# Kernel optimization log

Hardware: AMD Instinct MI355X
Metric: run time of the kernel (lower is better)

## Reference

```python
import jax, jax.numpy as jnp
import numpy as np

B, C, T, COLS = 256, 1, 128, 512
IN_DIM = C * COLS          # 512
EMB = 1024
HID = 1024
NUM_LAYERS = 2
NUM_CLASSES = 10


def setup_inputs() -> dict:
    key = jax.random.key(0)
    ks = jax.random.split(key, 16)
    s = 0.05
    inp = {
        "x": jax.random.normal(ks[0], (B, C, T, COLS), dtype=jnp.float32),
        "W_enc": jax.random.normal(ks[1], (EMB, IN_DIM), dtype=jnp.float32) * s,
        "b_enc": jnp.zeros((EMB,), dtype=jnp.float32),
        # layer 0: input size EMB
        "W_ih0": jax.random.normal(ks[2], (4 * HID, EMB), dtype=jnp.float32) * s,
        "W_hh0": jax.random.normal(ks[3], (4 * HID, HID), dtype=jnp.float32) * s,
        "b_ih0": jnp.zeros((4 * HID,), dtype=jnp.float32),
        "b_hh0": jnp.zeros((4 * HID,), dtype=jnp.float32),
        # layer 1: input size HID
        "W_ih1": jax.random.normal(ks[4], (4 * HID, HID), dtype=jnp.float32) * s,
        "W_hh1": jax.random.normal(ks[5], (4 * HID, HID), dtype=jnp.float32) * s,
        "b_ih1": jnp.zeros((4 * HID,), dtype=jnp.float32),
        "b_hh1": jnp.zeros((4 * HID,), dtype=jnp.float32),
        "W_cls": jax.random.normal(ks[6], (NUM_CLASSES, HID), dtype=jnp.float32) * s,
        "b_cls": jnp.zeros((NUM_CLASSES,), dtype=jnp.float32),
    }
    return inp


def _lstm_cell(x, h, c, W_ih, W_hh, b_ih, b_hh):
    # gates: [B, 4H], PyTorch gate order i, f, g, o
    gates = x @ W_ih.T + b_ih + h @ W_hh.T + b_hh
    i, f, g, o = jnp.split(gates, 4, axis=-1)
    i = jax.nn.sigmoid(i)
    f = jax.nn.sigmoid(f)
    g = jnp.tanh(g)
    o = jax.nn.sigmoid(o)
    c_new = f * c + i * g
    h_new = o * jnp.tanh(c_new)
    return h_new, c_new


def reference(x, W_enc, b_enc, W_ih0, W_hh0, b_ih0, b_hh0,
              W_ih1, W_hh1, b_ih1, b_hh1, W_cls, b_cls):
    b_size = x.shape[0]
    # [B, C, T, COLS] -> [B, T, C*COLS]
    x_rowed = x.reshape(b_size, T, IN_DIM)
    emb = x_rowed @ W_enc.T + b_enc            # [B, T, EMB]
    emb_t = jnp.transpose(emb, (1, 0, 2))      # [T, B, EMB]

    layer_params = [(W_ih0, W_hh0, b_ih0, b_hh0), (W_ih1, W_hh1, b_ih1, b_hh1)]
    h0 = jnp.zeros((NUM_LAYERS, b_size, HID), dtype=x.dtype)
    c0 = jnp.zeros((NUM_LAYERS, b_size, HID), dtype=x.dtype)

    def step(carry, x_t):
        h, c = carry  # each [L, B, H]
        inp = x_t
        hs, cs = [], []
        for l in range(NUM_LAYERS):
            h_l, c_l = _lstm_cell(inp, h[l], c[l], *layer_params[l])
            hs.append(h_l)
            cs.append(c_l)
            inp = h_l
        return (jnp.stack(hs), jnp.stack(cs)), inp

    (_, _), outs = jax.lax.scan(step, (h0, c0), emb_t)  # outs: [T, B, H]
    last = outs[-1]                                     # [B, H]
    y = last @ W_cls.T + b_cls                          # [B, 10]
    return y
```

## Files before the change

kernel.cpp:

```cpp
#include <hip/hip_runtime.h>

#define B_SZ   256
#define T_SZ   128
#define IN_DIM 512
#define EMB    1024
#define HID    1024
#define G4     4096
#define NCLS   10
#define PSTR   2560
#define NBLK   256

typedef __attribute__((ext_vector_type(8))) short short8v;
typedef __attribute__((ext_vector_type(4))) float floatx4;

__device__ __forceinline__ unsigned short bf16hi(float f) {
    union { float f; unsigned u; } v; v.f = f;
    unsigned r = v.u + 0x7fff + ((v.u >> 16) & 1);
    return (unsigned short)(r >> 16);
}
__device__ __forceinline__ float bf2f(unsigned short b) {
    union { unsigned u; float f; } v; v.u = ((unsigned)b) << 16;
    return v.f;
}

#define LGKM0_BAR()  do { \
    asm volatile("s_waitcnt lgkmcnt(0)" ::: "memory"); \
    __builtin_amdgcn_sched_barrier(0); \
    __builtin_amdgcn_s_barrier(); \
    __builtin_amdgcn_sched_barrier(0); } while (0)

template<int BM,int BN,int BK,int TM,int TN>
__global__ __launch_bounds__((BM/TM)*(BN/TN))
void gemm_f32_nn(const float* __restrict__ A, const float* __restrict__ Bm,
                 float* __restrict__ C, int M, int N, int K) {
    constexpr int THREADS = (BM/TM)*(BN/TN);
    __shared__ float As[BK][BM+4];
    __shared__ float Bs[BK][BN+4];
    const int tid  = threadIdx.x;
    const int tcol = tid % (BN/TN);
    const int trow = tid / (BN/TN);
    const int bm   = blockIdx.y * BM;
    const int bn   = blockIdx.x * BN;
    float acc[TM][TN];
#pragma unroll
    for (int i = 0; i < TM; ++i)
#pragma unroll
        for (int j = 0; j < TN; ++j) acc[i][j] = 0.f;
    for (int k0 = 0; k0 < K; k0 += BK) {
#pragma unroll
        for (int r = 0; r < BM*BK/4; r += THREADS) {
            int i  = r + tid;
            int m  = i / (BK/4);
            int kk = (i % (BK/4)) * 4;
            const float4 v = *(const float4*)(&A[(size_t)(bm+m)*K + k0 + kk]);
            As[kk+0][m]=v.x; As[kk+1][m]=v.y; As[kk+2][m]=v.z; As[kk+3][m]=v.w;
        }
#pragma unroll
        for (int r = 0; r < BK*BN/4; r += THREADS) {
            int i  = r + tid;
            int kk = i / (BN/4);
            int n4 = (i % (BN/4)) * 4;
            const float4 v = *(const float4*)(&Bm[(size_t)(k0+kk)*N + bn + n4]);
            *(float4*)(&Bs[kk][n4]) = v;
        }
        __syncthreads();
#pragma unroll
        for (int k = 0; k < BK; ++k) {
            float a[TM], b[TN];
#pragma unroll
            for (int i = 0; i < TM; ++i) a[i] = As[k][trow*TM+i];
#pragma unroll
            for (int j = 0; j < TN; ++j) b[j] = Bs[k][tcol*TN+j];
#pragma unroll
            for (int i = 0; i < TM; ++i)
#pragma unroll
                for (int j = 0; j < TN; ++j) acc[i][j] += a[i]*b[j];
        }
        __syncthreads();
    }
#pragma unroll
    for (int i = 0; i < TM; ++i)
#pragma unroll
        for (int j = 0; j < TN; ++j)
            C[(size_t)(bm+trow*TM+i)*N + bn + tcol*TN + j] = acc[i][j];
}

__global__ void swz2(const float* __restrict__ M0, int K0, int kf0,
                     const float* __restrict__ M1, int K1, int kfcnt,
                     unsigned short* __restrict__ dst) {
    int gid = blockIdx.x * 256 + threadIdx.x;
    int l   = gid & 63;
    int kf  = (gid >> 6) % kfcnt;
    int cf  = gid / (64 * kfcnt);
    int n   = cf*16 + (l & 15);
    int row = ((n & 3) << 10) + (n >> 2);
    const float* src; int kk = (l >> 4) * 8;
    if (kf < kf0) { src = M0 + (size_t)row * K0; kk += kf * 32; }
    else          { src = M1 + (size_t)row * K1; kk += (kf - kf0) * 32; }
    short8v vh, vl;
#pragma unroll
    for (int j = 0; j < 8; ++j) {
        float f = src[kk + j];
        unsigned short h = bf16hi(f);
        vh[j] = (short)h;
        vl[j] = (short)bf16hi(f - bf2f(h));
    }
    size_t base = ((size_t)(cf * kfcnt + kf) * 2) * 512 + (size_t)l * 8;
    *(short8v*)(dst + base)       = vh;
    *(short8v*)(dst + base + 512) = vl;
}

__global__ void build_bcombI(const float* __restrict__ W_ih0, const float* __restrict__ b_enc,
                             const float* __restrict__ b_ih0, const float* __restrict__ b_hh0,
                             float* __restrict__ bcombI) {
    int row  = blockIdx.x * 4 + (threadIdx.x >> 6);
    int lane = threadIdx.x & 63;
    const float* w = W_ih0 + (size_t)row * EMB;
    float s = 0.f;
    for (int k = lane; k < EMB; k += 64) s += w[k] * b_enc[k];
#pragma unroll
    for (int o = 32; o > 0; o >>= 1) s += __shfl_down(s, o);
    if (lane == 0) {
        int n = ((row & 1023) << 2) | (row >> 10);
        bcombI[n] = s + b_ih0[row] + b_hh0[row];
    }
}

__global__ void addvI(const float* __restrict__ a, const float* __restrict__ b,
                      float* __restrict__ o) {
    int i = blockIdx.x * 256 + threadIdx.x;
    int n = ((i & 1023) << 2) | (i >> 10);
    o[n] = a[i] + b[i];
}

__device__ __forceinline__ void gridbar(unsigned* bar, unsigned target, int tid) {
    __syncthreads();
    if (tid == 0) {
        __threadfence();
        atomicAdd(bar, 1u);
        while (__hip_atomic_load(bar, __ATOMIC_RELAXED, __HIP_MEMORY_SCOPE_AGENT) < target)
            __builtin_amdgcn_s_sleep(1);
        __threadfence();
    }
    __syncthreads();
}

__device__ __forceinline__ void store_xz(unsigned short* ph, unsigned short* pl,
                                         int bid, int tid, float2 xv) {
    unsigned short h0 = bf16hi(xv.x), h1 = bf16hi(xv.y);
    ushort2 hh; hh.x = h0; hh.y = h1;
    ushort2 lv; lv.x = bf16hi(xv.x - bf2f(h0)); lv.y = bf16hi(xv.y - bf2f(h1));
    size_t o = (size_t)bid * PSTR + tid * 2;
    *(ushort2*)(ph + o) = hh;
    *(ushort2*)(pl + o) = lv;
}

__global__ __launch_bounds__(512, 1)
void lstm_persist(const float* __restrict__ x,
                  const unsigned short* __restrict__ WLz,
                  const unsigned short* __restrict__ WRz,
                  const float* __restrict__ biasLI, const float* __restrict__ biasRI,
                  unsigned short* __restrict__ p0h, unsigned short* __restrict__ p0l,
                  unsigned short* __restrict__ p1h, unsigned short* __restrict__ p1l,
                  const float* __restrict__ Wcls, const float* __restrict__ bcls,
                  float* __restrict__ out, unsigned* __restrict__ bar) {
    __shared__ unsigned short AslH[32768];
    float (*gtile)[68] = (float (*)[68])AslH;

    const int tid = threadIdx.x, bid = blockIdx.x;
    const int w = tid >> 6, l = tid & 63;
    const int kgrp = w >> 2, sub = w & 3;
    const int rowhalf = sub & 1, colhalf = sub >> 1;
    const int xcd = bid & 7;
    const int idx = bid >> 3;
    const bool is_left = (idx < 16);
    const int i2 = is_left ? idx : idx - 16;
    const int cgl = xcd * 8 + (i2 & 7);
    const int rg  = i2 >> 3;
    const int kfcnt = is_left ? 48 : 64;
    const int SMAXH = is_left ? 24 : 32;
    const int acol0 = is_left ? 0 : 512;
    const int hcol0 = is_left ? 512 : 1536;
    const int r0 = rg * 128;
    const unsigned short* Bz = is_left ? WLz : WRz;
    const float* biasI = is_left ? biasLI : biasRI;
    const int kf_base = kgrp * SMAXH;
    const int NS = SMAXH;

    const int cf0 = cgl*4 + colhalf*2;
    const unsigned short* bp0 = Bz + ((size_t)cf0     * kfcnt) * 1024 + (size_t)l * 8;
    const unsigned short* bp1 = Bz + ((size_t)(cf0+1) * kfcnt) * 1024 + (size_t)l * 8;

    float bias0 = 0.f, bias1 = 0.f;
    if (kgrp == 0) {
        int cA = cgl*64 + colhalf*32 + (l & 15);
        bias0 = biasI[cA]; bias1 = biasI[cA + 16];
    }

    unsigned short* PH[2] = {p0h, p1h};
    unsigned short* PL[2] = {p0l, p1l};

    float cst[4];
#pragma unroll
    for (int i = 0; i < 4; ++i) cst[i] = 0.f;

    unsigned target = 0;

    if (tid < 256) {
        float2 xv = *(const float2*)&x[((size_t)bid * T_SZ) * IN_DIM + tid * 2];
        store_xz(p0h, p0l, bid, tid, xv);
    }
    target += NBLK; gridbar(bar, target, tid);

    for (int t = 0; t <= T_SZ; ++t) {
        const int cur = t & 1, nxt = cur ^ 1;
        const bool conv = (t < T_SZ - 1) && (tid < 256);
        float2 xv;
        if (conv) xv = *(const float2*)&x[((size_t)bid * T_SZ + t + 1) * IN_DIM + tid * 2];

        const bool active = is_left ? (t < T_SZ) : (t >= 1);
        if (active) {
            const unsigned short* ph  = PH[cur];
            const unsigned short* plo = PL[cur];

            auto loadA = [&](int s, short8v (&r)[4]) {
#pragma unroll
                for (int i = 0; i < 4; ++i) {
                    int seg = w*4 + i;
                    int kg = seg >> 4, mf = (seg >> 1) & 7, pl = seg & 1;
                    int kf = kg * SMAXH + s;
                    const unsigned short* p = pl ? plo : ph;
                    size_t o = (size_t)(r0 + mf*16 + (l & 15)) * PSTR
                             + acol0 + kf*32 + ((l >> 4) * 8);
                    r[i] = *(const short8v*)(p + o);
                }
            };
            auto writeA = [&](int buf, short8v (&r)[4]) {
#pragma unroll
                for (int i = 0; i < 4; ++i) {
                    int seg = w*4 + i;
                    int kg = seg >> 4, mf = (seg >> 1) & 7, pl = seg & 1;
                    *(short8v*)(AslH + (size_t)((((buf*2 + kg)*8 + mf)*2 + pl)*64 + l)*8) = r[i];
                }
            };
            auto loadB = [&](int s, short8v (&b)[4]) {
                int kf = kf_base + s;
                const unsigned short* q0 = bp0 + (size_t)kf * 1024;
                const unsigned short* q1 = bp1 + (size_t)kf * 1024;
                b[0] = *(const short8v*)q0; b[1] = *(const short8v*)(q0 + 512);
                b[2] = *(const short8v*)q1; b[3] = *(const short8v*)(q1 + 512);
            };

            floatx4 acc[4][2];
#pragma unroll
            for (int m = 0; m < 4; ++m) {
                acc[m][0] = (floatx4){bias0, bias0, bias0, bias0};
                acc[m][1] = (floatx4){bias1, bias1, bias1, bias1};
            }

            auto mfmaStage = [&](int buf, short8v (&b)[4]) {
                short8v ah[4], al[4];
#pragma unroll
                for (int m = 0; m < 4; ++m) {
                    size_t base = (size_t)((((buf*2 + kgrp)*8 + rowhalf*4 + m)*2)*64 + l)*8;
                    ah[m] = *(const short8v*)(AslH + base);
                    al[m] = *(const short8v*)(AslH + base + 512);
                }
#pragma unroll
                for (int m = 0; m < 4; ++m) {
                    acc[m][0] = __builtin_amdgcn_mfma_f32_16x16x32_bf16(ah[m], b[0], acc[m][0], 0, 0, 0);
                    acc[m][0] = __builtin_amdgcn_mfma_f32_16x16x32_bf16(ah[m], b[1], acc[m][0], 0, 0, 0);
                    acc[m][0] = __builtin_amdgcn_mfma_f32_16x16x32_bf16(al[m], b[0], acc[m][0], 0, 0, 0);
                    acc[m][1] = __builtin_amdgcn_mfma_f32_16x16x32_bf16(ah[m], b[2], acc[m][1], 0, 0, 0);
                    acc[m][1] = __builtin_amdgcn_mfma_f32_16x16x32_bf16(ah[m], b[3], acc[m][1], 0, 0, 0);
                    acc[m][1] = __builtin_amdgcn_mfma_f32_16x16x32_bf16(al[m], b[2], acc[m][1], 0, 0, 0);
                }
            };

            short8v rA[4], rB[4], bE[4], bO[4];
            loadA(0, rA); loadB(0, bE);
            loadA(1, rB); loadB(1, bO);
            writeA(0, rA);
            LGKM0_BAR();

            for (int s = 0; s < NS; s += 2) {
                if (s + 2 < NS) loadA(s + 2, rA);
                writeA(1, rB);
                mfmaStage(0, bE);
                if (s + 2 < NS) loadB(s + 2, bE);
                LGKM0_BAR();
                if (s + 3 < NS) loadA(s + 3, rB);
                if (s + 2 < NS) writeA(0, rA);
                mfmaStage(1, bO);
                if (s + 3 < NS) loadB(s + 3, bO);
                LGKM0_BAR();
            }
            __syncthreads();

            if (kgrp == 0) {
#pragma unroll
                for (int m = 0; m < 4; ++m)
#pragma unroll
                    for (int c = 0; c < 2; ++c) {
                        int col = colhalf*32 + c*16 + (l & 15);
#pragma unroll
                        for (int jj = 0; jj < 4; ++jj)
                            gtile[rowhalf*64 + m*16 + ((l >> 4)*4) + jj][col] = acc[m][c][jj];
                    }
            }
            __syncthreads();
            if (kgrp == 1) {
#pragma unroll
                for (int m = 0; m < 4; ++m)
#pragma unroll
                    for (int c = 0; c < 2; ++c) {
                        int col = colhalf*32 + c*16 + (l & 15);
#pragma unroll
                        for (int jj = 0; jj < 4; ++jj)
                            gtile[rowhalf*64 + m*16 + ((l >> 4)*4) + jj][col] += acc[m][c][jj];
                    }
            }
            __syncthreads();

            {
                int u = tid & 15, rq = tid >> 4;
                unsigned short* nh = PH[nxt];
                unsigned short* nl = PL[nxt];
#pragma unroll
                for (int i = 0; i < 4; ++i) {
                    int r = rq*4 + i;
                    float4 gq = *(const float4*)&gtile[r][4*u];
                    float ii = 1.f / (1.f + expf(-gq.x));
                    float ff = 1.f / (1.f + expf(-gq.y));
                    float gg = tanhf(gq.z);
                    float oo = 1.f / (1.f + expf(-gq.w));
                    float cn = ff * cst[i] + ii * gg;
                    cst[i] = cn;
                    float h = oo * tanhf(cn);
                    unsigned short hh = bf16hi(h);
                    size_t o = (size_t)(r0 + r) * PSTR + hcol0 + cgl*16 + u;
                    nh[o] = hh;
                    nl[o] = bf16hi(h - bf2f(hh));
                }
            }
        }

        if (conv) store_xz(PH[nxt], PL[nxt], bid, tid, xv);
        target += NBLK; gridbar(bar, target, tid);
    }

    {
        const unsigned short* hh = PH[(T_SZ + 1) & 1];
        const unsigned short* hl = PL[(T_SZ + 1) & 1];
        float part[NCLS];
#pragma unroll
        for (int n = 0; n < NCLS; ++n) part[n] = 0.f;
        for (int k = tid; k < HID; k += 512) {
            size_t o = (size_t)bid * PSTR + 1536 + k;
            float hv = bf2f(hh[o]) + bf2f(hl[o]);
#pragma unroll
            for (int n = 0; n < NCLS; ++n) part[n] += hv * Wcls[(size_t)n * HID + k];
        }
        float* red = (float*)AslH;
        for (int n = 0; n < NCLS; ++n) {
            red[tid] = part[n];
            __syncthreads();
            for (int s = 256; s > 0; s >>= 1) {
                if (tid < s) red[tid] += red[tid + s];
                __syncthreads();
            }
            if (tid == 0) out[(size_t)bid * NCLS + n] = red[0] + bcls[n];
            __syncthreads();
        }
    }
}

extern "C" void kernel_launch(void* const* d_in, const int* in_sizes, int n_in,
                              void* d_out, int out_size, void* d_ws, size_t ws_size,
                              hipStream_t stream) {
    const float* x      = (const float*)d_in[0];
    const float* W_enc  = (const float*)d_in[1];
    const float* b_enc  = (const float*)d_in[2];
    const float* W_ih0  = (const float*)d_in[3];
    const float* W_hh0  = (const float*)d_in[4];
    const float* b_ih0  = (const float*)d_in[5];
    const float* b_hh0  = (const float*)d_in[6];
    const float* W_ih1  = (const float*)d_in[7];
    const float* W_hh1  = (const float*)d_in[8];
    const float* b_ih1  = (const float*)d_in[9];
    const float* b_hh1  = (const float*)d_in[10];
    const float* W_cls  = (const float*)d_in[11];
    const float* b_cls  = (const float*)d_in[12];
    float* out = (float*)d_out;

    float* ws = (float*)d_ws;
    size_t off = 0;
    unsigned short* WLz    = (unsigned short*)(ws + off); off += (size_t)G4 * 1536 * 2 / 2;
    unsigned short* WRz    = (unsigned short*)(ws + off); off += (size_t)G4 * 2048 * 2 / 2;
    float*          Wcomb  = ws + off;                    off += (size_t)G4 * IN_DIM;
    float*          biasLI = ws + off;                    off += G4;
    float*          biasRI = ws + off;                    off += G4;
    unsigned short* planes = (unsigned short*)(ws + off); off += (size_t)4 * B_SZ * PSTR / 2;
    unsigned*       bar    = (unsigned*)(ws + off);       off += 64;

    unsigned short* p0h = planes;
    unsigned short* p0l = p0h + (size_t)B_SZ * PSTR;
    unsigned short* p1h = p0l + (size_t)B_SZ * PSTR;
    unsigned short* p1l = p1h + (size_t)B_SZ * PSTR;

    gemm_f32_nn<128,128,16,8,8><<<dim3(IN_DIM/128, G4/128), 256, 0, stream>>>(
        W_ih0, W_enc, Wcomb, G4, IN_DIM, EMB);
    build_bcombI<<<G4/4, 256, 0, stream>>>(W_ih0, b_enc, b_ih0, b_hh0, biasLI);
    addvI<<<G4/256, 256, 0, stream>>>(b_ih1, b_hh1, biasRI);
    swz2<<<64*48, 256, 0, stream>>>(Wcomb, IN_DIM, 16, W_hh0, HID, 48, WLz);
    swz2<<<64*64, 256, 0, stream>>>(W_ih1, HID, 32, W_hh1, HID, 64, WRz);
    hipMemsetAsync(planes, 0, (size_t)4 * B_SZ * PSTR * 2, stream);
    hipMemsetAsync(bar, 0, sizeof(unsigned), stream);

    lstm_persist<<<NBLK, 512, 0, stream>>>(
        x, WLz, WRz, biasLI, biasRI,
        p0h, p0l, p1h, p1l, W_cls, b_cls, out, bar);
}
```

Before: 9.103 ms.

## Split K-groups across separate blocks with global partial-sum handoff via flags

The persistent LSTM kernel now runs 512 blocks of 256 threads, two per CU, instead of 256 blocks of 512 threads. The two K-halves of each output tile that previously shared one block now run in separate blocks. The kgrp 0 block writes its partial accumulators to a global scratch buffer and signals a per-tile flag, and the kgrp 1 block spins on that flag, adds the partials and applies the LSTM cell update. MFMA sections get raised wave priority, and the LDS waitcnt barriers become plain __syncthreads. This aims to improve occupancy and latency hiding, at the cost of extra global traffic, flag spin latency and a grid barrier with twice as many participants.

```diff
diff --git a/kernel.cpp b/kernel.cpp
--- a/kernel.cpp
+++ b/kernel.cpp
@@ -8,7 +8,7 @@
 #define G4     4096
 #define NCLS   10
 #define PSTR   2560
-#define NBLK   256
+#define NBLK   512
 
 typedef __attribute__((ext_vector_type(8))) short short8v;
 typedef __attribute__((ext_vector_type(4))) float floatx4;
@@ -22,12 +22,6 @@
     union { unsigned u; float f; } v; v.u = ((unsigned)b) << 16;
     return v.f;
 }
-
-#define LGKM0_BAR()  do { \
-    asm volatile("s_waitcnt lgkmcnt(0)" ::: "memory"); \
-    __builtin_amdgcn_sched_barrier(0); \
-    __builtin_amdgcn_s_barrier(); \
-    __builtin_amdgcn_sched_barrier(0); } while (0)
 
 template<int BM,int BN,int BK,int TM,int TN>
 __global__ __launch_bounds__((BM/TM)*(BN/TN))
@@ -155,7 +149,7 @@
     *(ushort2*)(pl + o) = lv;
 }
 
-__global__ __launch_bounds__(512, 1)
+__global__ __launch_bounds__(256, 2)
 void lstm_persist(const float* __restrict__ x,
                   const unsigned short* __restrict__ WLz,
                   const unsigned short* __restrict__ WRz,
@@ -163,29 +157,33 @@
                   unsigned short* __restrict__ p0h, unsigned short* __restrict__ p0l,
                   unsigned short* __restrict__ p1h, unsigned short* __restrict__ p1l,
                   const float* __restrict__ Wcls, const float* __restrict__ bcls,
-                  float* __restrict__ out, unsigned* __restrict__ bar) {
-    __shared__ unsigned short AslH[32768];
-    float (*gtile)[68] = (float (*)[68])AslH;
+                  float* __restrict__ out, unsigned* __restrict__ bar,
+                  unsigned* __restrict__ flags, float* __restrict__ gpart) {
+    __shared__ float smem[128 * 68];
+    unsigned short* AslH = (unsigned short*)smem;
+    float (*gtile)[68] = (float (*)[68])smem;
 
     const int tid = threadIdx.x, bid = blockIdx.x;
     const int w = tid >> 6, l = tid & 63;
-    const int kgrp = w >> 2, sub = w & 3;
-    const int rowhalf = sub & 1, colhalf = sub >> 1;
+    const int rowhalf = w & 1, colhalf = w >> 1;
     const int xcd = bid & 7;
     const int idx = bid >> 3;
-    const bool is_left = (idx < 16);
-    const int i2 = is_left ? idx : idx - 16;
-    const int cgl = xcd * 8 + (i2 & 7);
-    const int rg  = i2 >> 3;
+    const int kgrp = idx & 1;
+    const int j = idx >> 1;
+    const bool is_left = (j < 16);
+    const int s4 = j & 15;
+    const int cgl = xcd * 8 + (s4 & 7);
+    const int rg  = s4 >> 3;
+    const int tile = j * 8 + xcd;
     const int kfcnt = is_left ? 48 : 64;
-    const int SMAXH = is_left ? 24 : 32;
+    const int SMAXH = kfcnt >> 1;
+    const int NS = SMAXH;
     const int acol0 = is_left ? 0 : 512;
     const int hcol0 = is_left ? 512 : 1536;
     const int r0 = rg * 128;
     const unsigned short* Bz = is_left ? WLz : WRz;
     const float* biasI = is_left ? biasLI : biasRI;
     const int kf_base = kgrp * SMAXH;
-    const int NS = SMAXH;
 
     const int cf0 = cgl*4 + colhalf*2;
     const unsigned short* bp0 = Bz + ((size_t)cf0     * kfcnt) * 1024 + (size_t)l * 8;
@@ -200,13 +198,14 @@
     unsigned short* PH[2] = {p0h, p1h};
     unsigned short* PL[2] = {p0l, p1l};
 
-    float cst[4];
-#pragma unroll
-    for (int i = 0; i < 4; ++i) cst[i] = 0.f;
+    float cst[8];
+#pragma unroll
+    for (int i = 0; i < 8; ++i) cst[i] = 0.f;
 
     unsigned target = 0;
-
-    if (tid < 256) {
+    unsigned myflag = 1;
+
+    if (bid < B_SZ) {
         float2 xv = *(const float2*)&x[((size_t)bid * T_SZ) * IN_DIM + tid * 2];
         store_xz(p0h, p0l, bid, tid, xv);
     }
@@ -214,7 +213,7 @@
 
     for (int t = 0; t <= T_SZ; ++t) {
         const int cur = t & 1, nxt = cur ^ 1;
-        const bool conv = (t < T_SZ - 1) && (tid < 256);
+        const bool conv = (t < T_SZ - 1) && (bid < B_SZ);
         float2 xv;
         if (conv) xv = *(const float2*)&x[((size_t)bid * T_SZ + t + 1) * IN_DIM + tid * 2];
 
@@ -227,8 +226,8 @@
 #pragma unroll
                 for (int i = 0; i < 4; ++i) {
                     int seg = w*4 + i;
-                    int kg = seg >> 4, mf = (seg >> 1) & 7, pl = seg & 1;
-                    int kf = kg * SMAXH + s;
+                    int mf = seg >> 1, pl = seg & 1;
+                    int kf = kf_base + s;
                     const unsigned short* p = pl ? plo : ph;
                     size_t o = (size_t)(r0 + mf*16 + (l & 15)) * PSTR
                              + acol0 + kf*32 + ((l >> 4) * 8);
@@ -239,8 +238,7 @@
 #pragma unroll
                 for (int i = 0; i < 4; ++i) {
                     int seg = w*4 + i;
-                    int kg = seg >> 4, mf = (seg >> 1) & 7, pl = seg & 1;
-                    *(short8v*)(AslH + (size_t)((((buf*2 + kg)*8 + mf)*2 + pl)*64 + l)*8) = r[i];
+                    *(short8v*)(AslH + (size_t)((buf*16 + seg)*64 + l)*8) = r[i];
                 }
             };
             auto loadB = [&](int s, short8v (&b)[4]) {
@@ -262,10 +260,11 @@
                 short8v ah[4], al[4];
 #pragma unroll
                 for (int m = 0; m < 4; ++m) {
-                    size_t base = (size_t)((((buf*2 + kgrp)*8 + rowhalf*4 + m)*2)*64 + l)*8;
+                    size_t base = (size_t)((buf*16 + (rowhalf*4 + m)*2)*64 + l)*8;
                     ah[m] = *(const short8v*)(AslH + base);
                     al[m] = *(const short8v*)(AslH + base + 512);
                 }
+                __builtin_amdgcn_s_setprio(1);
 #pragma unroll
                 for (int m = 0; m < 4; ++m) {
                     acc[m][0] = __builtin_amdgcn_mfma_f32_16x16x32_bf16(ah[m], b[0], acc[m][0], 0, 0, 0);
@@ -275,29 +274,64 @@
                     acc[m][1] = __builtin_amdgcn_mfma_f32_16x16x32_bf16(ah[m], b[3], acc[m][1], 0, 0, 0);
                     acc[m][1] = __builtin_amdgcn_mfma_f32_16x16x32_bf16(al[m], b[2], acc[m][1], 0, 0, 0);
                 }
+                __builtin_amdgcn_s_setprio(0);
             };
 
             short8v rA[4], rB[4], bE[4], bO[4];
             loadA(0, rA); loadB(0, bE);
             loadA(1, rB); loadB(1, bO);
             writeA(0, rA);
-            LGKM0_BAR();
+            __syncthreads();
 
             for (int s = 0; s < NS; s += 2) {
                 if (s + 2 < NS) loadA(s + 2, rA);
                 writeA(1, rB);
                 mfmaStage(0, bE);
                 if (s + 2 < NS) loadB(s + 2, bE);
-                LGKM0_BAR();
+                __syncthreads();
                 if (s + 3 < NS) loadA(s + 3, rB);
                 if (s + 2 < NS) writeA(0, rA);
                 mfmaStage(1, bO);
                 if (s + 3 < NS) loadB(s + 3, bO);
-                LGKM0_BAR();
+                __syncthreads();
             }
-            __syncthreads();
 
             if (kgrp == 0) {
+                float* gp = gpart + (size_t)tile * 8192;
+#pragma unroll
+                for (int m = 0; m < 4; ++m)
+#pragma unroll
+                    for (int c = 0; c < 2; ++c) {
+                        int col = colhalf*32 + c*16 + (l & 15);
+#pragma unroll
+                        for (int jj = 0; jj < 4; ++jj) {
+                            int row = rowhalf*64 + m*16 + ((l >> 4)*4) + jj;
+                            gp[row*64 + col] = acc[m][c][jj];
+                        }
+                    }
+                __threadfence();
+                __syncthreads();
+                if (tid == 0) atomicAdd(&flags[tile*16], 1u);
+            } else {
+                if (tid == 0) {
+                    while (__hip_atomic_load(&flags[tile*16], __ATOMIC_RELAXED,
+                                             __HIP_MEMORY_SCOPE_AGENT) < myflag)
+                        __builtin_amdgcn_s_sleep(1);
+                }
+                __syncthreads();
+                __threadfence();
+                const float* gp = gpart + (size_t)tile * 8192;
+#pragma unroll
+                for (int m = 0; m < 4; ++m)
+#pragma unroll
+                    for (int c = 0; c < 2; ++c) {
+                        int col = colhalf*32 + c*16 + (l & 15);
+#pragma unroll
+                        for (int jj = 0; jj < 4; ++jj) {
+                            int row = rowhalf*64 + m*16 + ((l >> 4)*4) + jj;
+                            acc[m][c][jj] += gp[row*64 + col];
+                        }
+                    }
 #pragma unroll
                 for (int m = 0; m < 4; ++m)
 #pragma unroll
@@ -307,41 +341,29 @@
                         for (int jj = 0; jj < 4; ++jj)
                             gtile[rowhalf*64 + m*16 + ((l >> 4)*4) + jj][col] = acc[m][c][jj];
                     }
-            }
-            __syncthreads();
-            if (kgrp == 1) {
-#pragma unroll
-                for (int m = 0; m < 4; ++m)
-#pragma unroll
-                    for (int c = 0; c < 2; ++c) {
-                        int col = colhalf*32 + c*16 + (l & 15);
-#pragma unroll
-                        for (int jj = 0; jj < 4; ++jj)
-                            gtile[rowhalf*64 + m*16 + ((l >> 4)*4) + jj][col] += acc[m][c][jj];
+                __syncthreads();
+                {
+                    int u = tid & 15, rq = tid >> 4;
+                    unsigned short* nh = PH[nxt];
+                    unsigned short* nl = PL[nxt];
+#pragma unroll
+                    for (int i = 0; i < 8; ++i) {
+                        int r = rq*8 + i;
+                        float4 gq = *(const float4*)&gtile[r][4*u];
+                        float ii = 1.f / (1.f + expf(-gq.x));
+                        float ff = 1.f / (1.f + expf(-gq.y));
+                        float gg = tanhf(gq.z);
+                        float oo = 1.f / (1.f + expf(-gq.w));
+                        float cn = ff * cst[i] + ii * gg;
+                        cst[i] = cn;
+                        float h = oo * tanhf(cn);
+                        unsigned short hh = bf16hi(h);
+                        size_t o = (size_t)(r0 + r) * PSTR + hcol0 + cgl*16 + u;
+                        nh[o] = hh;
+                        nl[o] = bf16hi(h - bf2f(hh));
                     }
-            }
-            __syncthreads();
-
-            {
-                int u = tid & 15, rq = tid >> 4;
-                unsigned short* nh = PH[nxt];
-                unsigned short* nl = PL[nxt];
-#pragma unroll
-                for (int i = 0; i < 4; ++i) {
-                    int r = rq*4 + i;
-                    float4 gq = *(const float4*)&gtile[r][4*u];
-                    float ii = 1.f / (1.f + expf(-gq.x));
-                    float ff = 1.f / (1.f + expf(-gq.y));
-                    float gg = tanhf(gq.z);
-                    float oo = 1.f / (1.f + expf(-gq.w));
-                    float cn = ff * cst[i] + ii * gg;
-                    cst[i] = cn;
-                    float h = oo * tanhf(cn);
-                    unsigned short hh = bf16hi(h);
-                    size_t o = (size_t)(r0 + r) * PSTR + hcol0 + cgl*16 + u;
-                    nh[o] = hh;
-                    nl[o] = bf16hi(h - bf2f(hh));
-                }
+                }
+                myflag++;
             }
         }
 
@@ -349,23 +371,23 @@
         target += NBLK; gridbar(bar, target, tid);
     }
 
-    {
+    if (bid < B_SZ) {
         const unsigned short* hh = PH[(T_SZ + 1) & 1];
         const unsigned short* hl = PL[(T_SZ + 1) & 1];
         float part[NCLS];
 #pragma unroll
         for (int n = 0; n < NCLS; ++n) part[n] = 0.f;
-        for (int k = tid; k < HID; k += 512) {
+        for (int k = tid; k < HID; k += 256) {
             size_t o = (size_t)bid * PSTR + 1536 + k;
             float hv = bf2f(hh[o]) + bf2f(hl[o]);
 #pragma unroll
             for (int n = 0; n < NCLS; ++n) part[n] += hv * Wcls[(size_t)n * HID + k];
         }
-        float* red = (float*)AslH;
+        float* red = (float*)smem;
         for (int n = 0; n < NCLS; ++n) {
             red[tid] = part[n];
             __syncthreads();
-            for (int s = 256; s > 0; s >>= 1) {
+            for (int s = 128; s > 0; s >>= 1) {
                 if (tid < s) red[tid] += red[tid + s];
                 __syncthreads();
             }
@@ -402,6 +424,8 @@
     float*          biasRI = ws + off;                    off += G4;
     unsigned short* planes = (unsigned short*)(ws + off); off += (size_t)4 * B_SZ * PSTR / 2;
     unsigned*       bar    = (unsigned*)(ws + off);       off += 64;
+    unsigned*       flags  = (unsigned*)(ws + off);       off += 256 * 16;
+    float*          gpart  = ws + off;                    off += (size_t)256 * 8192;
 
     unsigned short* p0h = planes;
     unsigned short* p0l = p0h + (size_t)B_SZ * PSTR;
@@ -415,9 +439,9 @@
     swz2<<<64*48, 256, 0, stream>>>(Wcomb, IN_DIM, 16, W_hh0, HID, 48, WLz);
     swz2<<<64*64, 256, 0, stream>>>(W_ih1, HID, 32, W_hh1, HID, 64, WRz);
     hipMemsetAsync(planes, 0, (size_t)4 * B_SZ * PSTR * 2, stream);
-    hipMemsetAsync(bar, 0, sizeof(unsigned), stream);
-
-    lstm_persist<<<NBLK, 512, 0, stream>>>(
+    hipMemsetAsync(bar, 0, (64 + 256 * 16) * sizeof(unsigned), stream);
+
+    lstm_persist<<<NBLK, 256, 0, stream>>>(
         x, WLz, WRz, biasLI, biasRI,
-        p0h, p0l, p1h, p1l, W_cls, b_cls, out, bar);
-}
+        p0h, p0l, p1h, p1l, W_cls, b_cls, out, bar, flags, gpart);
+}
```

Measured after the change: 18.98 ms. 108% more time.

## Double persistent grid to 512 blocks with half-width column tiles per block

Applied to the files above, without the earlier changes.

The persistent LSTM kernel now runs 512 blocks instead of 256. Each block covers 32 gate columns instead of 64, so per-block MFMA work, B-fragment loads and LDS footprint are halved, and launch bounds allow several blocks per CU. The lgkmcnt-wait barriers are replaced by plain __syncthreads, and s_setprio is raised around the MFMA bursts. The intent is to shorten the per-timestep critical path by spreading work over more CUs. In exchange the grid barrier must synchronise twice as many blocks, and every block still reloads the full A tile of h from global memory each step.

```diff
diff --git a/kernel.cpp b/kernel.cpp
--- a/kernel.cpp
+++ b/kernel.cpp
@@ -8,7 +8,7 @@
 #define G4     4096
 #define NCLS   10
 #define PSTR   2560
-#define NBLK   256
+#define NBLK   512
 
 typedef __attribute__((ext_vector_type(8))) short short8v;
 typedef __attribute__((ext_vector_type(4))) float floatx4;
@@ -22,12 +22,6 @@
     union { unsigned u; float f; } v; v.u = ((unsigned)b) << 16;
     return v.f;
 }
-
-#define LGKM0_BAR()  do { \
-    asm volatile("s_waitcnt lgkmcnt(0)" ::: "memory"); \
-    __builtin_amdgcn_sched_barrier(0); \
-    __builtin_amdgcn_s_barrier(); \
-    __builtin_amdgcn_sched_barrier(0); } while (0)
 
 template<int BM,int BN,int BK,int TM,int TN>
 __global__ __launch_bounds__((BM/TM)*(BN/TN))
@@ -155,7 +149,7 @@
     *(ushort2*)(pl + o) = lv;
 }
 
-__global__ __launch_bounds__(512, 1)
+__global__ __launch_bounds__(512, 4)
 void lstm_persist(const float* __restrict__ x,
                   const unsigned short* __restrict__ WLz,
                   const unsigned short* __restrict__ WRz,
@@ -164,8 +158,8 @@
                   unsigned short* __restrict__ p1h, unsigned short* __restrict__ p1l,
                   const float* __restrict__ Wcls, const float* __restrict__ bcls,
                   float* __restrict__ out, unsigned* __restrict__ bar) {
-    __shared__ unsigned short AslH[32768];
-    float (*gtile)[68] = (float (*)[68])AslH;
+    __shared__ unsigned short AslH[2][32][64][8];
+    float (*gtile)[36] = (float (*)[36])AslH;
 
     const int tid = threadIdx.x, bid = blockIdx.x;
     const int w = tid >> 6, l = tid & 63;
@@ -173,40 +167,34 @@
     const int rowhalf = sub & 1, colhalf = sub >> 1;
     const int xcd = bid & 7;
     const int idx = bid >> 3;
-    const bool is_left = (idx < 16);
-    const int i2 = is_left ? idx : idx - 16;
-    const int cgl = xcd * 8 + (i2 & 7);
-    const int rg  = i2 >> 3;
+    const bool is_left = (idx < 32);
+    const int i2 = idx & 31;
+    const int cgl = xcd * 16 + (i2 & 15);
+    const int rg  = i2 >> 4;
     const int kfcnt = is_left ? 48 : 64;
-    const int SMAXH = is_left ? 24 : 32;
+    const int SMAXH = kfcnt >> 1;
+    const int NS = SMAXH;
     const int acol0 = is_left ? 0 : 512;
     const int hcol0 = is_left ? 512 : 1536;
     const int r0 = rg * 128;
     const unsigned short* Bz = is_left ? WLz : WRz;
     const float* biasI = is_left ? biasLI : biasRI;
     const int kf_base = kgrp * SMAXH;
-    const int NS = SMAXH;
-
-    const int cf0 = cgl*4 + colhalf*2;
-    const unsigned short* bp0 = Bz + ((size_t)cf0     * kfcnt) * 1024 + (size_t)l * 8;
-    const unsigned short* bp1 = Bz + ((size_t)(cf0+1) * kfcnt) * 1024 + (size_t)l * 8;
-
-    float bias0 = 0.f, bias1 = 0.f;
-    if (kgrp == 0) {
-        int cA = cgl*64 + colhalf*32 + (l & 15);
-        bias0 = biasI[cA]; bias1 = biasI[cA + 16];
-    }
+
+    const int cf = cgl*2 + colhalf;
+    const unsigned short* bp = Bz + ((size_t)cf * kfcnt) * 1024 + (size_t)l * 8;
+
+    float biasv = 0.f;
+    if (kgrp == 0) biasv = biasI[cgl*32 + colhalf*16 + (l & 15)];
 
     unsigned short* PH[2] = {p0h, p1h};
     unsigned short* PL[2] = {p0l, p1l};
 
-    float cst[4];
-#pragma unroll
-    for (int i = 0; i < 4; ++i) cst[i] = 0.f;
+    float cst[2] = {0.f, 0.f};
 
     unsigned target = 0;
 
-    if (tid < 256) {
+    if (bid < B_SZ && tid < 256) {
         float2 xv = *(const float2*)&x[((size_t)bid * T_SZ) * IN_DIM + tid * 2];
         store_xz(p0h, p0l, bid, tid, xv);
     }
@@ -214,7 +202,7 @@
 
     for (int t = 0; t <= T_SZ; ++t) {
         const int cur = t & 1, nxt = cur ^ 1;
-        const bool conv = (t < T_SZ - 1) && (tid < 256);
+        const bool conv = (t < T_SZ - 1) && (bid < B_SZ) && (tid < 256);
         float2 xv;
         if (conv) xv = *(const float2*)&x[((size_t)bid * T_SZ + t + 1) * IN_DIM + tid * 2];
 
@@ -239,96 +227,84 @@
 #pragma unroll
                 for (int i = 0; i < 4; ++i) {
                     int seg = w*4 + i;
-                    int kg = seg >> 4, mf = (seg >> 1) & 7, pl = seg & 1;
-                    *(short8v*)(AslH + (size_t)((((buf*2 + kg)*8 + mf)*2 + pl)*64 + l)*8) = r[i];
+                    *(short8v*)&AslH[buf][seg][l][0] = r[i];
                 }
             };
-            auto loadB = [&](int s, short8v (&b)[4]) {
-                int kf = kf_base + s;
-                const unsigned short* q0 = bp0 + (size_t)kf * 1024;
-                const unsigned short* q1 = bp1 + (size_t)kf * 1024;
-                b[0] = *(const short8v*)q0; b[1] = *(const short8v*)(q0 + 512);
-                b[2] = *(const short8v*)q1; b[3] = *(const short8v*)(q1 + 512);
+            auto loadB = [&](int s, short8v (&b)[2]) {
+                const unsigned short* q = bp + (size_t)(kf_base + s) * 1024;
+                b[0] = *(const short8v*)q;
+                b[1] = *(const short8v*)(q + 512);
             };
 
-            floatx4 acc[4][2];
-#pragma unroll
-            for (int m = 0; m < 4; ++m) {
-                acc[m][0] = (floatx4){bias0, bias0, bias0, bias0};
-                acc[m][1] = (floatx4){bias1, bias1, bias1, bias1};
-            }
-
-            auto mfmaStage = [&](int buf, short8v (&b)[4]) {
+            floatx4 acc[4];
+#pragma unroll
+            for (int m = 0; m < 4; ++m) acc[m] = (floatx4){biasv, biasv, biasv, biasv};
+
+            auto mfmaStage = [&](int buf, short8v (&b)[2]) {
                 short8v ah[4], al[4];
 #pragma unroll
                 for (int m = 0; m < 4; ++m) {
-                    size_t base = (size_t)((((buf*2 + kgrp)*8 + rowhalf*4 + m)*2)*64 + l)*8;
-                    ah[m] = *(const short8v*)(AslH + base);
-                    al[m] = *(const short8v*)(AslH + base + 512);
-                }
+                    int mf = rowhalf*4 + m;
+                    ah[m] = *(const short8v*)&AslH[buf][kgrp*16 + mf*2 + 0][l][0];
+                    al[m] = *(const short8v*)&AslH[buf][kgrp*16 + mf*2 + 1][l][0];
+                }
+                __builtin_amdgcn_s_setprio(1);
 #pragma unroll
                 for (int m = 0; m < 4; ++m) {
-                    acc[m][0] = __builtin_amdgcn_mfma_f32_16x16x32_bf16(ah[m], b[0], acc[m][0], 0, 0, 0);
-                    acc[m][0] = __builtin_amdgcn_mfma_f32_16x16x32_bf16(ah[m], b[1], acc[m][0], 0, 0, 0);
-                    acc[m][0] = __builtin_amdgcn_mfma_f32_16x16x32_bf16(al[m], b[0], acc[m][0], 0, 0, 0);
-                    acc[m][1] = __builtin_amdgcn_mfma_f32_16x16x32_bf16(ah[m], b[2], acc[m][1], 0, 0, 0);
-                    acc[m][1] = __builtin_amdgcn_mfma_f32_16x16x32_bf16(ah[m], b[3], acc[m][1], 0, 0, 0);
-                    acc[m][1] = __builtin_amdgcn_mfma_f32_16x16x32_bf16(al[m], b[2], acc[m][1], 0, 0, 0);
-                }
+                    acc[m] = __builtin_amdgcn_mfma_f32_16x16x32_bf16(ah[m], b[0], acc[m], 0, 0, 0);
+                    acc[m] = __builtin_amdgcn_mfma_f32_16x16x32_bf16(ah[m], b[1], acc[m], 0, 0, 0);
+                    acc[m] = __builtin_amdgcn_mfma_f32_16x16x32_bf16(al[m], b[0], acc[m], 0, 0, 0);
+                }
+                __builtin_amdgcn_s_setprio(0);
             };
 
-            short8v rA[4], rB[4], bE[4], bO[4];
+            short8v rA[4], rB[4], bE[2], bO[2];
             loadA(0, rA); loadB(0, bE);
             loadA(1, rB); loadB(1, bO);
             writeA(0, rA);
-            LGKM0_BAR();
+            __syncthreads();
 
             for (int s = 0; s < NS; s += 2) {
                 if (s + 2 < NS) loadA(s + 2, rA);
                 writeA(1, rB);
                 mfmaStage(0, bE);
                 if (s + 2 < NS) loadB(s + 2, bE);
-                LGKM0_BAR();
+                __syncthreads();
                 if (s + 3 < NS) loadA(s + 3, rB);
                 if (s + 2 < NS) writeA(0, rA);
                 mfmaStage(1, bO);
                 if (s + 3 < NS) loadB(s + 3, bO);
-                LGKM0_BAR();
-            }
-            __syncthreads();
+                __syncthreads();
+            }
 
             if (kgrp == 0) {
 #pragma unroll
-                for (int m = 0; m < 4; ++m)
-#pragma unroll
-                    for (int c = 0; c < 2; ++c) {
-                        int col = colhalf*32 + c*16 + (l & 15);
-#pragma unroll
-                        for (int jj = 0; jj < 4; ++jj)
-                            gtile[rowhalf*64 + m*16 + ((l >> 4)*4) + jj][col] = acc[m][c][jj];
-                    }
+                for (int m = 0; m < 4; ++m) {
+                    int col = colhalf*16 + (l & 15);
+#pragma unroll
+                    for (int jj = 0; jj < 4; ++jj)
+                        gtile[rowhalf*64 + m*16 + ((l >> 4)*4) + jj][col] = acc[m][jj];
+                }
             }
             __syncthreads();
             if (kgrp == 1) {
 #pragma unroll
-                for (int m = 0; m < 4; ++m)
-#pragma unroll
-                    for (int c = 0; c < 2; ++c) {
-                        int col = colhalf*32 + c*16 + (l & 15);
-#pragma unroll
-                        for (int jj = 0; jj < 4; ++jj)
-                            gtile[rowhalf*64 + m*16 + ((l >> 4)*4) + jj][col] += acc[m][c][jj];
-                    }
+                for (int m = 0; m < 4; ++m) {
+                    int col = colhalf*16 + (l & 15);
+#pragma unroll
+                    for (int jj = 0; jj < 4; ++jj)
+                        gtile[rowhalf*64 + m*16 + ((l >> 4)*4) + jj][col] += acc[m][jj];
+                }
             }
             __syncthreads();
 
             {
-                int u = tid & 15, rq = tid >> 4;
+                int u = tid & 7, rq = tid >> 3;
                 unsigned short* nh = PH[nxt];
                 unsigned short* nl = PL[nxt];
 #pragma unroll
-                for (int i = 0; i < 4; ++i) {
-                    int r = rq*4 + i;
+                for (int i = 0; i < 2; ++i) {
+                    int r = rq*2 + i;
                     float4 gq = *(const float4*)&gtile[r][4*u];
                     float ii = 1.f / (1.f + expf(-gq.x));
                     float ff = 1.f / (1.f + expf(-gq.y));
@@ -338,7 +314,7 @@
                     cst[i] = cn;
                     float h = oo * tanhf(cn);
                     unsigned short hh = bf16hi(h);
-                    size_t o = (size_t)(r0 + r) * PSTR + hcol0 + cgl*16 + u;
+                    size_t o = (size_t)(r0 + r) * PSTR + hcol0 + cgl*8 + u;
                     nh[o] = hh;
                     nl[o] = bf16hi(h - bf2f(hh));
                 }
@@ -349,7 +325,7 @@
         target += NBLK; gridbar(bar, target, tid);
     }
 
-    {
+    if (bid < B_SZ) {
         const unsigned short* hh = PH[(T_SZ + 1) & 1];
         const unsigned short* hl = PL[(T_SZ + 1) & 1];
         float part[NCLS];
@@ -415,7 +391,7 @@
     swz2<<<64*48, 256, 0, stream>>>(Wcomb, IN_DIM, 16, W_hh0, HID, 48, WLz);
     swz2<<<64*64, 256, 0, stream>>>(W_ih1, HID, 32, W_hh1, HID, 64, WRz);
     hipMemsetAsync(planes, 0, (size_t)4 * B_SZ * PSTR * 2, stream);
-    hipMemsetAsync(bar, 0, sizeof(unsigned), stream);
+    hipMemsetAsync(bar, 0, 64 * sizeof(unsigned), stream);
 
     lstm_persist<<<NBLK, 512, 0, stream>>>(
         x, WLz, WRz, biasLI, biasRI,
```

New measurement: 15.48 ms. 1.7x slower.
